# Kernel tuning notes

Measured on AMD Instinct MI355X. Metric: run time of the kernel, lower is better.

## Reference

```python
import jax, jax.numpy as jnp
import numpy as np

B, T, C = 4, 4096, 512
H = 64           # head_size
GRAN = 128       # staircase granularity


def staircase_mask(t, g):
    # tril OR block-diagonal blocks of size g (the staircase fills the upper
    # triangle inside each gxg diagonal block)
    i = jnp.arange(t)
    return (i[:, None] >= i[None, :]) | ((i[:, None] // g) == (i[None, :] // g))


def setup_inputs() -> dict:
    key = jax.random.key(0)
    kx, kk, kq, kv = jax.random.split(key, 4)
    scale = 0.02
    return {
        "x": jax.random.normal(kx, (B, T, C), dtype=jnp.float32),
        "Wk": jax.random.normal(kk, (C, H), dtype=jnp.float32) * scale,
        "Wq": jax.random.normal(kq, (C, H), dtype=jnp.float32) * scale,
        "Wv": jax.random.normal(kv, (C, H), dtype=jnp.float32) * scale,
    }


def reference(x, Wk, Wq, Wv):
    # single head of self-attention with staircase mask (dropout off / eval mode)
    k = x @ Wk          # [B,T,H]
    q = x @ Wq          # [B,T,H]
    v = x @ Wv          # [B,T,H]
    wei = jnp.einsum("bth,bsh->bts", q, k) * (H ** -0.5)   # [B,T,T]
    mask = staircase_mask(T, GRAN)                           # [T,T] bool
    wei = jnp.where(mask, wei, -jnp.inf)
    wei = jax.nn.softmax(wei, axis=-1)
    out = jnp.einsum("bts,bsh->bth", wei, v)                 # [B,T,H]
    return out
```

## Files before the change

kernel.cpp:

```cpp
#include <hip/hip_runtime.h>

typedef unsigned short u16;
typedef unsigned int u32;
typedef unsigned long long u64;
typedef __attribute__((ext_vector_type(8))) short short8;
typedef __attribute__((ext_vector_type(4))) float f32x4;

#define T_ 4096
#define QSCALE 0.18033688f
#define CH 4
#define SBAT 576
#define PSTRIDE 36

#if __has_builtin(__builtin_amdgcn_exp2f)
#define EXP2F(x) __builtin_amdgcn_exp2f(x)
#else
#define EXP2F(x) exp2f(x)
#endif

__device__ __forceinline__ u16 f2bf(float f) {
    unsigned u = __float_as_uint(f);
    u += 0x7FFFu + ((u >> 16) & 1u);
    return (u16)(u >> 16);
}

__global__ __launch_bounds__(256) void wtrans_kernel(
    const float* __restrict__ Wq, const float* __restrict__ Wk,
    const float* __restrict__ Wv, u16* __restrict__ WTf)
{
    const int tid  = blockIdx.x * 256 + threadIdx.x;
    const int frag = tid >> 6;
    const int lane = tid & 63;
    const int ng   = frag >> 4;
    const int kc   = frag & 15;
    const int m    = ng >> 2;
    const float* W = (m == 0) ? Wq : (m == 1) ? Wk : Wv;
    const int h  = (ng & 3) * 16 + (lane & 15);
    const int c0 = kc * 32 + (lane >> 4) * 8;
    short8 v;
    #pragma unroll
    for (int j = 0; j < 8; ++j)
        v[j] = (short)f2bf(W[(c0 + j) * 64 + h]);
    *(short8*)(WTf + (size_t)frag * 512 + lane * 8) = v;
}

__global__ __launch_bounds__(256) void proj_kernel(
    const float* __restrict__ x, const u16* __restrict__ WTf,
    u16* __restrict__ Qf, u16* __restrict__ Kf, u16* __restrict__ Vf)
{
    __shared__ u16 xs[16 * 520];
    __shared__ u16 img[3072];
    const int t    = threadIdx.x;
    const int lane = t & 63;
    const int w    = t >> 6;
    const int l16  = lane & 15;
    const int quad = lane >> 4;
    const int rowbase = blockIdx.x * 16;
    const int bat  = rowbase >> 12;
    const int tloc = rowbase & 4095;

    #pragma unroll
    for (int it = 0; it < 8; ++it) {
        int f   = t + it * 256;
        int row = f >> 7;
        int c4  = (f & 127) * 4;
        f32x4 a = *(const f32x4*)(x + (size_t)(rowbase + row) * 512 + c4);
        unsigned lo = (unsigned)f2bf(a[0]) | ((unsigned)f2bf(a[1]) << 16);
        unsigned hi = (unsigned)f2bf(a[2]) | ((unsigned)f2bf(a[3]) << 16);
        *(uint2*)(xs + row * 520 + c4) = make_uint2(lo, hi);
    }
    __syncthreads();

    f32x4 acc[3];
    #pragma unroll
    for (int nt = 0; nt < 3; ++nt) acc[nt] = (f32x4){0.f, 0.f, 0.f, 0.f};

    const u16* ab = xs + l16 * 520 + quad * 8;
    const u16* wb = WTf + (size_t)(w * 3 * 16) * 512 + lane * 8;

    #pragma unroll 4
    for (int kc = 0; kc < 16; ++kc) {
        short8 af = *(const short8*)(ab + kc * 32);
        #pragma unroll
        for (int nt = 0; nt < 3; ++nt) {
            short8 bf = *(const short8*)(wb + (size_t)(nt * 16 + kc) * 512);
            acc[nt] = __builtin_amdgcn_mfma_f32_16x16x32_bf16(af, bf, acc[nt], 0, 0, 0);
        }
    }

    #pragma unroll
    for (int nt = 0; nt < 3; ++nt) {
        int ng = w * 3 + nt;
        if (ng < 8) {
            int ng4  = ng & 3;
            float sc = (ng < 4) ? QSCALE : 1.0f;
            u16* ib  = img + ((ng < 4) ? 0 : 1024) + (ng4 >> 1) * 512
                          + ((ng4 & 1) * 2 + (l16 >> 3)) * 128 + (l16 & 7);
            #pragma unroll
            for (int i = 0; i < 4; ++i)
                ib[(quad * 4 + i) * 8] = f2bf(acc[nt][i] * sc);
        } else {
            int nt2  = ng - 8;
            unsigned lo = (unsigned)f2bf(acc[nt][0]) | ((unsigned)f2bf(acc[nt][1]) << 16);
            unsigned hi = (unsigned)f2bf(acc[nt][2]) | ((unsigned)f2bf(acc[nt][3]) << 16);
            *(uint2*)(img + 2048 + nt2 * 256 + (quad >> 1) * 128 + l16 * 8
                          + (quad & 1) * 4) = make_uint2(lo, hi);
        }
    }
    __syncthreads();

    const int tb   = tloc >> 4;
    const int kt   = tloc >> 7;
    const int ks   = (tloc >> 5) & 3;
    const int half = (tloc >> 4) & 1;
    uint2 vq = *(uint2*)(img + t * 4);
    uint2 vk = *(uint2*)(img + 1024 + t * 4);
    uint2 vv = *(uint2*)(img + 2048 + t * 4);
    *(uint2*)(Qf + (size_t)(bat * 256 + tb) * 1024 + t * 4) = vq;
    *(uint2*)(Kf + (size_t)(bat * 256 + tb) * 1024 + t * 4) = vk;
    const int nt2c = t >> 6;
    *(uint2*)(Vf + (size_t)((bat * 32 + kt) * 4 + ks) * 2048
                 + nt2c * 512 + half * 256 + (t & 63) * 4) = vv;
}

__global__ __launch_bounds__(256, 4) void attn_kernel(
    const u16* __restrict__ Qf, const u16* __restrict__ Kf,
    const u16* __restrict__ Vf, u32* __restrict__ pnum,
    float* __restrict__ pden, float* __restrict__ out)
{
    __shared__ u16 Ps[4][2][16 * PSTRIDE];

    const int w    = threadIdx.x >> 6;
    const int lane = threadIdx.x & 63;
    const int l16  = lane & 15;
    const int qd   = lane >> 4;
    const int xcd  = blockIdx.x & 7;
    const int bat  = xcd >> 1;
    const int tw   = ((blockIdx.x >> 3) * 2 + (xcd & 1)) * 4 + w;

    int A = 31, pre = 0, cc = 1;
    for (;;) {
        cc = (A + CH) / CH;
        int cnt4 = 4 * cc;
        if (tw < pre + cnt4) break;
        pre += cnt4; --A;
    }
    const int r    = tw - pre;
    const int c    = r >> 2;
    const int b_   = r & 3;
    const int nkt  = A + 1;
    const int q32  = 4 * A + b_;
    const int kt0  = c * CH;
    const int kt1  = min(kt0 + CH, nkt);
    const int slot = bat * SBAT + pre + b_ + 4 * c;

    short8 aq[2][2];
    #pragma unroll
    for (int g = 0; g < 2; ++g)
        #pragma unroll
        for (int f = 0; f < 2; ++f)
            aq[g][f] = *(const short8*)(Qf
                + ((size_t)((bat * 256 + q32 * 2 + g) * 2 + f)) * 512 + lane * 8);

    short8 ones;
    #pragma unroll
    for (int j = 0; j < 8; ++j) ones[j] = (short)0x3F80;

    f32x4 acc[2][4];
    f32x4 accden[2];
    #pragma unroll
    for (int g = 0; g < 2; ++g) {
        accden[g] = (f32x4){0.f, 0.f, 0.f, 0.f};
        for (int n = 0; n < 4; ++n) acc[g][n] = (f32x4){0.f, 0.f, 0.f, 0.f};
    }

    u16* Pw[2] = { &Ps[w][0][0], &Ps[w][1][0] };

    auto body = [&](int kt) __attribute__((always_inline)) {
        const u16* kfb = Kf + ((size_t)(bat * 256 + kt * 8) * 2) * 512 + lane * 8;
        const u16* vfb = Vf + ((size_t)((bat * 32 + kt) * 16)) * 512 + lane * 8;
        #pragma unroll
        for (int ks = 0; ks < 4; ++ks) {
            #pragma unroll
            for (int b = 0; b < 2; ++b) {
                int nt = 2 * ks + b;
                short8 k0 = *(const short8*)(kfb + (size_t)nt * 1024);
                short8 k1 = *(const short8*)(kfb + (size_t)nt * 1024 + 512);
                #pragma unroll
                for (int g = 0; g < 2; ++g) {
                    f32x4 st = (f32x4){0.f, 0.f, 0.f, 0.f};
                    st = __builtin_amdgcn_mfma_f32_16x16x32_bf16(k0, aq[g][0], st, 0, 0, 0);
                    st = __builtin_amdgcn_mfma_f32_16x16x32_bf16(k1, aq[g][1], st, 0, 0, 0);
                    float p0 = EXP2F(st[0]);
                    float p1 = EXP2F(st[1]);
                    float p2 = EXP2F(st[2]);
                    float p3 = EXP2F(st[3]);
                    u32 q01 = __builtin_amdgcn_perm(__float_as_uint(p1), __float_as_uint(p0), 0x07060302u);
                    u32 q23 = __builtin_amdgcn_perm(__float_as_uint(p3), __float_as_uint(p2), 0x07060302u);
                    u64 pv = (u64)q01 | ((u64)q23 << 32);
                    *(u64*)(Pw[g] + l16 * PSTRIDE + b * 16 + qd * 4) = pv;
                }
            }
            short8 ap[2];
            #pragma unroll
            for (int g = 0; g < 2; ++g)
                ap[g] = *(const short8*)(Pw[g] + l16 * PSTRIDE + qd * 8);
            accden[0] = __builtin_amdgcn_mfma_f32_16x16x32_bf16(ones, ap[0], accden[0], 0, 0, 0);
            accden[1] = __builtin_amdgcn_mfma_f32_16x16x32_bf16(ones, ap[1], accden[1], 0, 0, 0);
            #pragma unroll
            for (int nt2 = 0; nt2 < 4; ++nt2) {
                short8 av = *(const short8*)(vfb + (size_t)(ks * 4 + nt2) * 512);
                acc[0][nt2] = __builtin_amdgcn_mfma_f32_16x16x32_bf16(av, ap[0], acc[0][nt2], 0, 0, 0);
                acc[1][nt2] = __builtin_amdgcn_mfma_f32_16x16x32_bf16(av, ap[1], acc[1][nt2], 0, 0, 0);
            }
        }
    };

    body(kt0);
    if (kt0 + 1 < kt1) body(kt0 + 1);
    if (kt0 + 2 < kt1) body(kt0 + 2);
    if (kt0 + 3 < kt1) body(kt0 + 3);

    float den[2] = { accden[0][0], accden[1][0] };

    if (cc == 1) {
        const float rd0 = 1.0f / den[0];
        const float rd1 = 1.0f / den[1];
        float* op = out + ((size_t)(bat * T_ + q32 * 32 + l16)) * 64 + qd * 4;
        #pragma unroll
        for (int g = 0; g < 2; ++g) {
            const float rd = g ? rd1 : rd0;
            #pragma unroll
            for (int nt2 = 0; nt2 < 4; ++nt2) {
                f32x4 v;
                #pragma unroll
                for (int i = 0; i < 4; ++i) v[i] = acc[g][nt2][i] * rd;
                *(f32x4*)(op + (size_t)g * 16 * 64 + nt2 * 16) = v;
            }
        }
    } else {
        u32* np = pnum + (size_t)slot * 1024;
        #pragma unroll
        for (int g = 0; g < 2; ++g)
            #pragma unroll
            for (int nt2 = 0; nt2 < 4; ++nt2) {
                u32 lo = (u32)f2bf(acc[g][nt2][0]) | ((u32)f2bf(acc[g][nt2][1]) << 16);
                u32 hi = (u32)f2bf(acc[g][nt2][2]) | ((u32)f2bf(acc[g][nt2][3]) << 16);
                u64 val = (u64)lo | ((u64)hi << 32);
                __builtin_nontemporal_store(val, (u64*)(np + (g * 4 + nt2) * 128 + lane * 2));
            }
        if (lane < 32)
            __builtin_nontemporal_store(den[lane >> 4],
                                        &pden[(size_t)slot * 32 + lane]);
    }
}

__global__ __launch_bounds__(256) void fin_kernel(
    const u32* __restrict__ pnum, const float* __restrict__ pden,
    float* __restrict__ out)
{
    __shared__ float sden[8][32];
    __shared__ float rden[32];
    const int blk  = blockIdx.x;
    const int xcd  = blk & 7;
    const int bat  = xcd >> 1;
    const int rest = blk >> 3;
    const int q32  = (rest & 63) * 2 + (xcd & 1);
    const int hh   = rest >> 6;
    const int A = q32 >> 2, b = q32 & 3;
    const int cc = (A + CH) / CH;
    if (cc == 1) return;
    int pre = 0;
    for (int j = 31; j > A; --j) pre += 4 * ((j + CH) / CH);
    const int base = bat * SBAT + pre + b;

    {
        const int md  = threadIdx.x & 31;
        const int grp = threadIdx.x >> 5;
        float d = 0.f;
        for (int ci = grp; ci < cc; ci += 8)
            d += pden[(size_t)(base + 4 * ci) * 32 + md];
        sden[grp][md] = d;
    }
    __syncthreads();
    if (threadIdx.x < 32) {
        float d = 0.f;
        #pragma unroll
        for (int g2 = 0; g2 < 8; ++g2) d += sden[g2][threadIdx.x];
        rden[threadIdx.x] = 1.0f / d;
    }
    __syncthreads();

    const int m   = threadIdx.x >> 3;
    const int g   = m >> 4;
    const int l16 = m & 15;
    const int h0  = hh * 32 + (threadIdx.x & 7) * 4;
    const int nt2 = h0 >> 4;
    const int q0  = (h0 >> 2) & 3;
    const int off = (g * 4 + nt2) * 128 + q0 * 32 + l16 * 2;

    float sv0 = 0.f, sv1 = 0.f, sv2 = 0.f, sv3 = 0.f;
    const u32* sp = pnum + (size_t)base * 1024 + off;
    uint2 cur = *(const uint2*)sp;
    for (int ci = 1; ci < cc; ++ci) {
        uint2 nxt = *(const uint2*)(sp + (size_t)ci * 4096);
        sv0 += __uint_as_float(cur.x << 16);
        sv1 += __uint_as_float(cur.x & 0xFFFF0000u);
        sv2 += __uint_as_float(cur.y << 16);
        sv3 += __uint_as_float(cur.y & 0xFFFF0000u);
        cur = nxt;
    }
    sv0 += __uint_as_float(cur.x << 16);
    sv1 += __uint_as_float(cur.x & 0xFFFF0000u);
    sv2 += __uint_as_float(cur.y << 16);
    sv3 += __uint_as_float(cur.y & 0xFFFF0000u);

    const float rd = rden[m];
    float* op = out + (size_t)(bat * T_ + q32 * 32 + m) * 64 + h0;
    f32x4 r;
    r[0] = sv0 * rd; r[1] = sv1 * rd; r[2] = sv2 * rd; r[3] = sv3 * rd;
    *(f32x4*)op = r;
}

extern "C" void kernel_launch(void* const* d_in, const int* in_sizes, int n_in,
                              void* d_out, int out_size, void* d_ws, size_t ws_size,
                              hipStream_t stream)
{
    const float* x  = (const float*)d_in[0];
    const float* Wk = (const float*)d_in[1];
    const float* Wq = (const float*)d_in[2];
    const float* Wv = (const float*)d_in[3];
    float* out = (float*)d_out;

    u16* ws  = (u16*)d_ws;
    u16* WTf = ws;
    u16* Qf  = ws + 131072;
    u16* Kf  = Qf + 1048576;
    u16* Vf  = Kf + 1048576;
    u32*   pnum = (u32*)(Vf + 1048576);
    float* pden = (float*)(pnum + (size_t)4 * 1088 * 1024);

    wtrans_kernel<<<48, 256, 0, stream>>>(Wq, Wk, Wv, WTf);
    proj_kernel<<<1024, 256, 0, stream>>>(x, WTf, Qf, Kf, Vf);
    attn_kernel<<<SBAT, 256, 0, stream>>>(Qf, Kf, Vf, pnum, pden, out);
    fin_kernel<<<1024, 256, 0, stream>>>(pnum, pden, out);
}
```

Measured before the change: 117.7 us.

## Software-pipeline QK and PV MFMAs across k-steps with double-buffered P tile

Restructures the inner attention loop so that the PV and denominator MFMAs for the previous 32-key step are issued after the current step's QK score MFMAs, while the current exp2 and LDS write proceed. P is double-buffered in shared memory by parity, and V fragments plus the P reload are carried in registers to the next step. The aim is to hide exp and LDS latency behind independent matrix work. The cost is more live registers (av_prev, ap_prev, four score tiles) and double the LDS for P, which could hurt occupancy at launch bounds of 4.

```diff
diff --git a/kernel.cpp b/kernel.cpp
--- a/kernel.cpp
+++ b/kernel.cpp
@@ -128,7 +128,7 @@
     const u16* __restrict__ Vf, u32* __restrict__ pnum,
     float* __restrict__ pden, float* __restrict__ out)
 {
-    __shared__ u16 Ps[4][2][16 * PSTRIDE];
+    __shared__ u16 Ps[4][2][2][16 * PSTRIDE];
 
     const int w    = threadIdx.x >> 6;
     const int lane = threadIdx.x & 63;
@@ -174,52 +174,95 @@
         for (int n = 0; n < 4; ++n) acc[g][n] = (f32x4){0.f, 0.f, 0.f, 0.f};
     }
 
-    u16* Pw[2] = { &Ps[w][0][0], &Ps[w][1][0] };
-
-    auto body = [&](int kt) __attribute__((always_inline)) {
+    u16* Psw = &Ps[w][0][0][0];
+    int par = 0;
+
+    short8 ap_prev[2];
+    short8 av_prev[4];
+
+    auto step = [&](int kt, int ks, bool first) __attribute__((always_inline)) {
         const u16* kfb = Kf + ((size_t)(bat * 256 + kt * 8) * 2) * 512 + lane * 8;
         const u16* vfb = Vf + ((size_t)((bat * 32 + kt) * 16)) * 512 + lane * 8;
-        #pragma unroll
-        for (int ks = 0; ks < 4; ++ks) {
-            #pragma unroll
-            for (int b = 0; b < 2; ++b) {
-                int nt = 2 * ks + b;
-                short8 k0 = *(const short8*)(kfb + (size_t)nt * 1024);
-                short8 k1 = *(const short8*)(kfb + (size_t)nt * 1024 + 512);
-                #pragma unroll
-                for (int g = 0; g < 2; ++g) {
-                    f32x4 st = (f32x4){0.f, 0.f, 0.f, 0.f};
-                    st = __builtin_amdgcn_mfma_f32_16x16x32_bf16(k0, aq[g][0], st, 0, 0, 0);
-                    st = __builtin_amdgcn_mfma_f32_16x16x32_bf16(k1, aq[g][1], st, 0, 0, 0);
-                    float p0 = EXP2F(st[0]);
-                    float p1 = EXP2F(st[1]);
-                    float p2 = EXP2F(st[2]);
-                    float p3 = EXP2F(st[3]);
-                    u32 q01 = __builtin_amdgcn_perm(__float_as_uint(p1), __float_as_uint(p0), 0x07060302u);
-                    u32 q23 = __builtin_amdgcn_perm(__float_as_uint(p3), __float_as_uint(p2), 0x07060302u);
-                    u64 pv = (u64)q01 | ((u64)q23 << 32);
-                    *(u64*)(Pw[g] + l16 * PSTRIDE + b * 16 + qd * 4) = pv;
-                }
+        f32x4 st0g0, st0g1, st1g0, st1g1;
+        {
+            short8 k0 = *(const short8*)(kfb + (size_t)(2 * ks) * 1024);
+            short8 k1 = *(const short8*)(kfb + (size_t)(2 * ks) * 1024 + 512);
+            f32x4 s;
+            s = (f32x4){0.f, 0.f, 0.f, 0.f};
+            s = __builtin_amdgcn_mfma_f32_16x16x32_bf16(k0, aq[0][0], s, 0, 0, 0);
+            s = __builtin_amdgcn_mfma_f32_16x16x32_bf16(k1, aq[0][1], s, 0, 0, 0);
+            st0g0 = s;
+            s = (f32x4){0.f, 0.f, 0.f, 0.f};
+            s = __builtin_amdgcn_mfma_f32_16x16x32_bf16(k0, aq[1][0], s, 0, 0, 0);
+            s = __builtin_amdgcn_mfma_f32_16x16x32_bf16(k1, aq[1][1], s, 0, 0, 0);
+            st0g1 = s;
+        }
+        {
+            short8 k0 = *(const short8*)(kfb + (size_t)(2 * ks + 1) * 1024);
+            short8 k1 = *(const short8*)(kfb + (size_t)(2 * ks + 1) * 1024 + 512);
+            f32x4 s;
+            s = (f32x4){0.f, 0.f, 0.f, 0.f};
+            s = __builtin_amdgcn_mfma_f32_16x16x32_bf16(k0, aq[0][0], s, 0, 0, 0);
+            s = __builtin_amdgcn_mfma_f32_16x16x32_bf16(k1, aq[0][1], s, 0, 0, 0);
+            st1g0 = s;
+            s = (f32x4){0.f, 0.f, 0.f, 0.f};
+            s = __builtin_amdgcn_mfma_f32_16x16x32_bf16(k0, aq[1][0], s, 0, 0, 0);
+            s = __builtin_amdgcn_mfma_f32_16x16x32_bf16(k1, aq[1][1], s, 0, 0, 0);
+            st1g1 = s;
+        }
+        if (!first) {
+            accden[0] = __builtin_amdgcn_mfma_f32_16x16x32_bf16(ones, ap_prev[0], accden[0], 0, 0, 0);
+            accden[1] = __builtin_amdgcn_mfma_f32_16x16x32_bf16(ones, ap_prev[1], accden[1], 0, 0, 0);
+            #pragma unroll
+            for (int nt2 = 0; nt2 < 4; ++nt2) {
+                acc[0][nt2] = __builtin_amdgcn_mfma_f32_16x16x32_bf16(av_prev[nt2], ap_prev[0], acc[0][nt2], 0, 0, 0);
+                acc[1][nt2] = __builtin_amdgcn_mfma_f32_16x16x32_bf16(av_prev[nt2], ap_prev[1], acc[1][nt2], 0, 0, 0);
             }
-            short8 ap[2];
-            #pragma unroll
-            for (int g = 0; g < 2; ++g)
-                ap[g] = *(const short8*)(Pw[g] + l16 * PSTRIDE + qd * 8);
-            accden[0] = __builtin_amdgcn_mfma_f32_16x16x32_bf16(ones, ap[0], accden[0], 0, 0, 0);
-            accden[1] = __builtin_amdgcn_mfma_f32_16x16x32_bf16(ones, ap[1], accden[1], 0, 0, 0);
-            #pragma unroll
-            for (int nt2 = 0; nt2 < 4; ++nt2) {
-                short8 av = *(const short8*)(vfb + (size_t)(ks * 4 + nt2) * 512);
-                acc[0][nt2] = __builtin_amdgcn_mfma_f32_16x16x32_bf16(av, ap[0], acc[0][nt2], 0, 0, 0);
-                acc[1][nt2] = __builtin_amdgcn_mfma_f32_16x16x32_bf16(av, ap[1], acc[1][nt2], 0, 0, 0);
+        }
+        u16* sw = Psw + par * 1152;
+        #pragma unroll
+        for (int b = 0; b < 2; ++b) {
+            #pragma unroll
+            for (int g = 0; g < 2; ++g) {
+                f32x4 s = (b == 0) ? (g == 0 ? st0g0 : st0g1)
+                                   : (g == 0 ? st1g0 : st1g1);
+                float p0 = EXP2F(s[0]);
+                float p1 = EXP2F(s[1]);
+                float p2 = EXP2F(s[2]);
+                float p3 = EXP2F(s[3]);
+                u32 q01 = __builtin_amdgcn_perm(__float_as_uint(p1), __float_as_uint(p0), 0x07060302u);
+                u32 q23 = __builtin_amdgcn_perm(__float_as_uint(p3), __float_as_uint(p2), 0x07060302u);
+                u64 pv = (u64)q01 | ((u64)q23 << 32);
+                *(u64*)(sw + g * 576 + l16 * PSTRIDE + b * 16 + qd * 4) = pv;
             }
         }
+        #pragma unroll
+        for (int nt2 = 0; nt2 < 4; ++nt2)
+            av_prev[nt2] = *(const short8*)(vfb + (size_t)(ks * 4 + nt2) * 512);
+        ap_prev[0] = *(const short8*)(sw + 0 * 576 + l16 * PSTRIDE + qd * 8);
+        ap_prev[1] = *(const short8*)(sw + 1 * 576 + l16 * PSTRIDE + qd * 8);
+        par ^= 1;
     };
 
-    body(kt0);
-    if (kt0 + 1 < kt1) body(kt0 + 1);
-    if (kt0 + 2 < kt1) body(kt0 + 2);
-    if (kt0 + 3 < kt1) body(kt0 + 3);
+    auto body = [&](int kt, bool firstb) __attribute__((always_inline)) {
+        step(kt, 0, firstb);
+        step(kt, 1, false);
+        step(kt, 2, false);
+        step(kt, 3, false);
+    };
+
+    body(kt0, true);
+    if (kt0 + 1 < kt1) body(kt0 + 1, false);
+    if (kt0 + 2 < kt1) body(kt0 + 2, false);
+    if (kt0 + 3 < kt1) body(kt0 + 3, false);
+
+    accden[0] = __builtin_amdgcn_mfma_f32_16x16x32_bf16(ones, ap_prev[0], accden[0], 0, 0, 0);
+    accden[1] = __builtin_amdgcn_mfma_f32_16x16x32_bf16(ones, ap_prev[1], accden[1], 0, 0, 0);
+    #pragma unroll
+    for (int nt2 = 0; nt2 < 4; ++nt2) {
+        acc[0][nt2] = __builtin_amdgcn_mfma_f32_16x16x32_bf16(av_prev[nt2], ap_prev[0], acc[0][nt2], 0, 0, 0);
+        acc[1][nt2] = __builtin_amdgcn_mfma_f32_16x16x32_bf16(av_prev[nt2], ap_prev[1], acc[1][nt2], 0, 0, 0);
+    }
 
     float den[2] = { accden[0][0], accden[1][0] };
 
```

New measurement: 116.8 us. No clear change (-0.7%).
